# Kernel tuning notes

Measured on AMD Instinct MI355X. Metric: run time of the kernel, lower is better.

## Reference

```python
import jax, jax.numpy as jnp
import numpy as np


def setup_inputs() -> dict:
    key = jax.random.key(0)
    k1, k2, k3, k4 = jax.random.split(key, 4)
    B, N, dim, heads, dim_head = 4, 1025, 768, 12, 64
    inner = heads * dim_head
    x = jax.random.normal(k1, (B, N, dim), dtype=jnp.float32)
    # binary occlusion mask over the N-1 patch tokens (CLS handled inside forward)
    mask = (jax.random.uniform(k2, (B, N - 1, dim)) > 0.5).astype(jnp.float32)
    w_qkv = jax.random.normal(k3, (inner * 3, dim), dtype=jnp.float32) * 0.02
    w_out = jax.random.normal(k4, (dim, inner), dtype=jnp.float32) * 0.02
    b_out = jnp.zeros((dim,), dtype=jnp.float32)
    return {"x": x, "mask": mask, "w_qkv": w_qkv, "w_out": w_out, "b_out": b_out, "heads": heads}


def reference(x, mask, w_qkv, w_out, b_out, heads):
    B, N, dim = x.shape
    inner = w_qkv.shape[0] // 3
    d = inner // heads
    scale = d ** -0.5

    def split_heads(t):  # [B, n, h*d] -> [B, h, n, d]
        return t.reshape(B, t.shape[1], heads, d).transpose(0, 2, 1, 3)

    qkv = x @ w_qkv.T  # [B, N, 3*inner]
    q, k, v = map(split_heads, jnp.split(qkv, 3, axis=-1))

    # --- mask propagation (torch.no_grad block) ---
    mask_sg = jax.lax.stop_gradient(mask)
    qkv_m = mask_sg @ jax.lax.stop_gradient(jnp.abs(w_qkv)).T  # [B, N-1, 3*inner]

    def norm_mask(t):
        t = split_heads(t)  # [B, h, N-1, d]
        t = t / (1e-6 + jnp.max(t, axis=2, keepdims=True))
        return jnp.concatenate([jnp.ones_like(t[:, :, :1]), t], axis=2)  # [B, h, N, d]

    q_m, k_m, v_m = map(norm_mask, jnp.split(qkv_m, 3, axis=-1))
    updated = (jnp.mean(mask_sg, axis=-1, keepdims=True) > 0.0).astype(x.dtype)  # [B, N-1, 1]
    updated = jnp.concatenate([jnp.ones_like(updated[:, :1]), updated], axis=1)  # [B, N, 1]

    # --- masked attention ---
    dots = jnp.einsum('bhnd,bhmd->bhnm', q * q_m, k * k_m) * scale
    attn = jax.nn.softmax(dots, axis=-1)
    out = jnp.einsum('bhnm,bhmd->bhnd', attn, v_m * v)
    out = out.transpose(0, 2, 1, 3).reshape(B, N, inner) * updated
    out = out @ w_out.T + b_out

    # --- mask output propagation (no grad) ---
    m = jax.lax.stop_gradient(jnp.einsum('bhnm,bhmd->bhnd', attn, v_m))
    m = m.transpose(0, 2, 1, 3).reshape(B, N, inner) * updated
    m = m @ jax.lax.stop_gradient(jnp.abs(w_out)).T
    return (out, m[:, 1:])
```

## Files before the change

kernel.cpp:

```cpp
#include <hip/hip_runtime.h>
#include <cmath>

#define TPB 256

static const int NTOK  = 1025;
static const int DIM   = 768;
static const int HEADS = 12;
static const int QK3   = 2304;
static const int ROWS  = 4 * NTOK;
static const int MROWS = 4 * (NTOK - 1);
static const int MPAD  = 4224;
static const int NPAD  = 1088;
static const size_t OUT0 = (size_t)ROWS * DIM;
static const size_t APLANE = (size_t)MPAD * DIM;

static const size_t OFF_QKV16  = 0;
static const size_t OFF_QKVM16 = 4800000;
static const size_t OFF_QE     = 9600000;
static const size_t OFF_KF     = 11300000;
static const size_t OFF_VF     = 13000000;
static const size_t OFF_ABF    = 16400000;
static const size_t OFF_WQ     = 19700000;
static const size_t OFF_WO     = 21500000;
static const size_t OFF_CMAX   = 22100000;
static const size_t OFF_UPD    = 22110000;

typedef __attribute__((ext_vector_type(8))) short short8;
typedef __attribute__((ext_vector_type(4))) float f32x4;

__device__ __forceinline__ unsigned short f2bf(float f) {
    union { float f; unsigned int u; } c; c.f = f;
    unsigned int u = c.u + 0x7fffu + ((c.u >> 16) & 1u);
    return (unsigned short)(u >> 16);
}
__device__ __forceinline__ float bf2f(unsigned short u) {
    union { unsigned int u; float f; } c; c.u = (unsigned int)u << 16;
    return c.f;
}
__device__ __forceinline__ unsigned int cvtpk(float a, float b) {
    unsigned int r;
    asm("v_cvt_pk_bf16_f32 %0, %1, %2" : "=v"(r) : "v"(a), "v"(b));
    return r;
}
__device__ __forceinline__ void gl_lds16(const unsigned short* g, unsigned short* l) {
    __builtin_amdgcn_global_load_lds(
        (const __attribute__((address_space(1))) unsigned int*)g,
        (__attribute__((address_space(3))) unsigned int*)l, 16, 0, 0);
}

__global__ __launch_bounds__(TPB)
void k_cvt(const float* __restrict__ x, const float* __restrict__ mask,
           const float* __restrict__ wqkv, const float* __restrict__ wout,
           unsigned short* __restrict__ Abf, unsigned short* __restrict__ Wq,
           unsigned short* __restrict__ Wo, float* __restrict__ upd,
           float* __restrict__ cmax)
{
    const int z = blockIdx.z;
    if (z == 4) {
        const int bx = blockIdx.x;
        if (bx == 0) {
            if (threadIdx.x < 4) upd[threadIdx.x * NTOK] = 1.f;
        } else if (bx < 10) {
            const int i4 = (bx - 1) * 256 + threadIdx.x;
            *(float4*)(cmax + (size_t)i4 * 4) = (float4){0.f, 0.f, 0.f, 0.f};
        }
        return;
    }
    const size_t idx = ((size_t)blockIdx.x * TPB + threadIdx.x) * 8;
    union { unsigned int u[4]; short8 s; } pk;
    if (z <= 1) {
        if (idx >= APLANE) return;
        const int row = (int)(idx / DIM);
        const int M = z ? MROWS : ROWS;
        const float* src = z ? mask : x;
        if (row < M) {
            float a[8];
            *(float4*)&a[0] = *(const float4*)(src + idx);
            *(float4*)&a[4] = *(const float4*)(src + idx + 4);
            pk.u[0] = cvtpk(a[0], a[1]); pk.u[1] = cvtpk(a[2], a[3]);
            pk.u[2] = cvtpk(a[4], a[5]); pk.u[3] = cvtpk(a[6], a[7]);
            if (z == 1) {
                const float s = ((a[0] + a[1]) + (a[2] + a[3])) + ((a[4] + a[5]) + (a[6] + a[7]));
                if (s > 0.f) {
                    const int b = row >> 10, j = row & 1023;
                    upd[b * NTOK + j + 1] = 1.f;
                }
            }
        } else {
            pk.u[0] = pk.u[1] = pk.u[2] = pk.u[3] = 0u;
        }
        *(short8*)(Abf + (size_t)z * APLANE + idx) = pk.s;
    } else {
        const size_t tot = (z == 2) ? (size_t)QK3 * DIM : (size_t)DIM * DIM;
        if (idx >= tot) return;
        const float* src = (z == 2) ? wqkv : wout;
        unsigned short* dst = (z == 2) ? Wq : Wo;
        float a[8];
        *(float4*)&a[0] = *(const float4*)(src + idx);
        *(float4*)&a[4] = *(const float4*)(src + idx + 4);
        union { unsigned int u[4]; short8 s; } pa;
        pk.u[0] = cvtpk(a[0], a[1]); pk.u[1] = cvtpk(a[2], a[3]);
        pk.u[2] = cvtpk(a[4], a[5]); pk.u[3] = cvtpk(a[6], a[7]);
#pragma unroll
        for (int i = 0; i < 4; ++i) pa.u[i] = pk.u[i] & 0x7FFF7FFFu;
        *(short8*)(dst + idx) = pk.s;
        *(short8*)(dst + tot + idx) = pa.s;
    }
}

__global__ __launch_bounds__(TPB)
void k_gemm_qkv_mfma(const unsigned short* __restrict__ Abf,
                     const unsigned short* __restrict__ Wq,
                     unsigned short* __restrict__ qkv16,
                     unsigned short* __restrict__ qkvm16,
                     float* __restrict__ cmax)
{
    const int bid = blockIdx.x;
    const int xcd = bid & 7, rr = bid >> 3;
    const int id = (xcd < 4) ? (xcd * 149 + rr) : (596 + (xcd - 4) * 148 + rr);
    const int z = id / 594;
    const int rem = id - z * 594;
    const int by = rem / 18, bx = rem - by * 18;
    const int rowT = by * 128, colT = bx * 128;
    if (z == 1 && rowT >= MROWS) return;
    const unsigned short* A = Abf + (size_t)z * APLANE;
    const unsigned short* B = Wq + (size_t)z * QK3 * DIM;

    __shared__ unsigned short As[2][128 * 64];
    __shared__ unsigned short Bs[2][128 * 64];

    const int t = threadIdx.x;
    const int w = t >> 6, lane = t & 63, l15 = lane & 15, quad = lane >> 4;
    const int wm = (w & 1) * 64, wn = (w >> 1) * 64;

    auto stage = [&](int buf, int k0) {
#pragma unroll
        for (int p = 0; p < 4; ++p) {
            const int i = p * 256 + t;
            const int row = i >> 3, ch = i & 7;
            const int gc = k0 + ((ch ^ (row & 7)) << 3);
            gl_lds16(A + (size_t)(rowT + row) * DIM + gc, As[buf] + (size_t)i * 8);
            gl_lds16(B + (size_t)(colT + row) * DIM + gc, Bs[buf] + (size_t)i * 8);
        }
    };

    f32x4 acc[4][4];
#pragma unroll
    for (int i = 0; i < 4; ++i)
#pragma unroll
        for (int j = 0; j < 4; ++j) acc[i][j] = (f32x4){0.f, 0.f, 0.f, 0.f};

    stage(0, 0);
#pragma clang loop unroll(disable)
    for (int kt = 0; kt < 12; ++kt) {
        const int cur = kt & 1;
        if (kt < 11) {
            stage(cur ^ 1, (kt + 1) * 64);
            asm volatile("s_waitcnt vmcnt(8)" ::: "memory");
        } else {
            asm volatile("s_waitcnt vmcnt(0)" ::: "memory");
        }
        __builtin_amdgcn_s_barrier();
        __builtin_amdgcn_sched_barrier(0);
        const unsigned short* as = As[cur];
        const unsigned short* bs = Bs[cur];
        short8 fa[2][4], fb[2][4];
#pragma unroll
        for (int kk = 0; kk < 2; ++kk) {
            const int rc = ((kk * 4 + quad) ^ (l15 & 7)) << 3;
#pragma unroll
            for (int mi = 0; mi < 4; ++mi) {
                fa[kk][mi] = *(const short8*)(as + (wm + mi * 16 + l15) * 64 + rc);
                fb[kk][mi] = *(const short8*)(bs + (wn + mi * 16 + l15) * 64 + rc);
            }
        }
        __builtin_amdgcn_s_setprio(1);
#pragma unroll
        for (int kk = 0; kk < 2; ++kk)
#pragma unroll
            for (int mi = 0; mi < 4; ++mi)
#pragma unroll
                for (int ni = 0; ni < 4; ++ni)
                    acc[mi][ni] = __builtin_amdgcn_mfma_f32_16x16x32_bf16(fa[kk][mi], fb[kk][ni], acc[mi][ni], 0, 0, 0);
        __builtin_amdgcn_s_setprio(0);
        asm volatile("s_waitcnt lgkmcnt(0)" ::: "memory");
        __builtin_amdgcn_s_barrier();
    }

    float cm[4] = {0.f, 0.f, 0.f, 0.f};
#pragma unroll
    for (int mi = 0; mi < 4; ++mi)
#pragma unroll
        for (int ni = 0; ni < 4; ++ni) {
            const int col = colT + wn + ni * 16 + l15;
#pragma unroll
            for (int r = 0; r < 4; ++r) {
                const int row = rowT + wm + mi * 16 + quad * 4 + r;
                const float v = acc[mi][ni][r];
                if (z == 0) {
                    if (row < ROWS) qkv16[(size_t)row * QK3 + col] = f2bf(v);
                } else {
                    qkvm16[(size_t)row * QK3 + col] = f2bf(v);
                    cm[ni] = fmaxf(cm[ni], v);
                }
            }
        }
    if (z == 1) {
        const int bb = rowT >> 10;
#pragma unroll
        for (int ni = 0; ni < 4; ++ni) {
            float m = cm[ni];
            m = fmaxf(m, __shfl_xor(m, 16, 64));
            m = fmaxf(m, __shfl_xor(m, 32, 64));
            if (quad == 0)
                atomicMax((int*)&cmax[bb * QK3 + colT + wn + ni * 16 + l15], __float_as_int(m));
        }
    }
}

__global__ __launch_bounds__(TPB)
void k_prep(const unsigned short* __restrict__ qkv16,
            const unsigned short* __restrict__ qkvm16,
            const float* __restrict__ cmax, unsigned short* __restrict__ qe,
            unsigned short* __restrict__ kfrag, unsigned short* __restrict__ vfrag)
{
    __shared__ unsigned short Vt_l[128 * 66];
    const int t = threadIdx.x;
    const int nt = blockIdx.x, h = blockIdx.y, b = blockIdx.z;
    const int bh = b * HEADS + h;
    const int nl = t >> 2, ds0 = (t & 3) * 16;
    const int n = nt * 64 + nl;
    const bool valid = n < NTOK;
    const int col0 = h * 64 + ds0;

    unsigned short q16[16] __attribute__((aligned(16))) = {0};
    unsigned short k16[16] __attribute__((aligned(16))) = {0};
    unsigned short v16[16] __attribute__((aligned(16))) = {0};
    unsigned short qm16[16] __attribute__((aligned(16)));
    unsigned short km16[16] __attribute__((aligned(16)));
    unsigned short vm16[16] __attribute__((aligned(16)));
    float cq[16], ck[16], cv[16];

    const bool useM = valid && (n > 0);
    if (valid) {
        const size_t br = (size_t)(b * NTOK + n) * QK3 + col0;
        *(short8*)&q16[0] = *(const short8*)(qkv16 + br);
        *(short8*)&q16[8] = *(const short8*)(qkv16 + br + 8);
        *(short8*)&k16[0] = *(const short8*)(qkv16 + br + 768);
        *(short8*)&k16[8] = *(const short8*)(qkv16 + br + 776);
        *(short8*)&v16[0] = *(const short8*)(qkv16 + br + 1536);
        *(short8*)&v16[8] = *(const short8*)(qkv16 + br + 1544);
    }
    if (useM) {
        const size_t mr = (size_t)(b * 1024 + (n - 1)) * QK3 + col0;
        *(short8*)&qm16[0] = *(const short8*)(qkvm16 + mr);
        *(short8*)&qm16[8] = *(const short8*)(qkvm16 + mr + 8);
        *(short8*)&km16[0] = *(const short8*)(qkvm16 + mr + 768);
        *(short8*)&km16[8] = *(const short8*)(qkvm16 + mr + 776);
        *(short8*)&vm16[0] = *(const short8*)(qkvm16 + mr + 1536);
        *(short8*)&vm16[8] = *(const short8*)(qkvm16 + mr + 1544);
        const int cb = b * QK3 + col0;
#pragma unroll
        for (int i = 0; i < 4; ++i) {
            *(float4*)&cq[i * 4] = *(const float4*)(cmax + cb + i * 4);
            *(float4*)&ck[i * 4] = *(const float4*)(cmax + cb + 768 + i * 4);
            *(float4*)&cv[i * 4] = *(const float4*)(cmax + cb + 1536 + i * 4);
        }
    }

    float fq[16], fk[16];
#pragma unroll
    for (int idx = 0; idx < 16; ++idx) {
        const float qm = useM ? bf2f(qm16[idx]) / (1e-6f + cq[idx]) : 1.f;
        const float km = useM ? bf2f(km16[idx]) / (1e-6f + ck[idx]) : 1.f;
        const float vm = valid ? (useM ? bf2f(vm16[idx]) / (1e-6f + cv[idx]) : 1.f) : 0.f;
        fq[idx] = bf2f(q16[idx]) * qm * 0.18033688f;
        fk[idx] = bf2f(k16[idx]) * km;
        const int d = ds0 + idx;
        Vt_l[d * 66 + nl]        = f2bf(bf2f(v16[idx]) * vm);
        Vt_l[(64 + d) * 66 + nl] = f2bf(vm);
    }
    union { unsigned int u[4]; short8 s; } pq0, pq1, pk0, pk1;
#pragma unroll
    for (int i = 0; i < 4; ++i) {
        pq0.u[i] = cvtpk(fq[2 * i],     fq[2 * i + 1]);
        pq1.u[i] = cvtpk(fq[8 + 2 * i], fq[9 + 2 * i]);
        pk0.u[i] = cvtpk(fk[2 * i],     fk[2 * i + 1]);
        pk1.u[i] = cvtpk(fk[8 + 2 * i], fk[9 + 2 * i]);
    }
    {
        unsigned short* qp = qe + ((size_t)bh * NPAD + n) * 64 + ds0;
        *(short8*)qp       = pq0.s;
        *(short8*)(qp + 8) = pq1.s;
    }
    {
        const int nc = nl >> 4, l15 = nl & 15;
        const int kk = ds0 >> 5, qb = (ds0 & 31) >> 3;
        unsigned short* kp = kfrag + (((size_t)bh * 17 + nt) * 8 + kk * 4 + nc) * 512;
        *(short8*)(kp + ((size_t)(qb * 16 + l15)) * 8)       = pk0.s;
        *(short8*)(kp + ((size_t)((qb + 1) * 16 + l15)) * 8) = pk1.s;
    }
    __syncthreads();
    const int c = t >> 1, nh = (t & 1) * 32;
    unsigned short ov[32] __attribute__((aligned(16)));
#pragma unroll
    for (int i = 0; i < 32; ++i) ov[i] = Vt_l[c * 66 + nh + i];
    const int c8 = c >> 4, l15v = c & 15, kkv = nh >> 5;
    unsigned short* vp = vfrag + (((size_t)bh * 17 + nt) * 16 + c8 * 2 + kkv) * 512 + (size_t)l15v * 8;
#pragma unroll
    for (int qd = 0; qd < 4; ++qd)
        *(short8*)(vp + (size_t)qd * 128) = *(short8*)(ov + qd * 8);
}

__global__ __launch_bounds__(64, 2)
void k_attn(const unsigned short* __restrict__ qe, const unsigned short* __restrict__ kfrag,
            const unsigned short* __restrict__ vfrag, const float* __restrict__ upd,
            unsigned short* __restrict__ ab2)
{
    const int flat = blockIdx.y * 33 + blockIdx.x;
    const int d2 = (flat & 7) * 198 + (flat >> 3);
    const int bh = d2 / 33, qt = d2 - bh * 33;
    const int b = bh / HEADS, h = bh - b * HEADS;
    const int lane = threadIdx.x;
    const int l15 = lane & 15, quad = lane >> 4;
    const int q0 = qt * 32;

    short8 qf[2][2];
#pragma unroll
    for (int j = 0; j < 2; ++j) {
        const unsigned short* qp = qe + ((size_t)bh * NPAD + q0 + j * 16 + l15) * 64 + (quad << 3);
        qf[j][0] = *(const short8*)qp;
        qf[j][1] = *(const short8*)(qp + 32);
    }
    const int pA = (quad & 1) * 32 + l15;
    const int pB = pA + 16;
    const bool lo32 = (lane < 32);

    const unsigned short* kb = kfrag + (size_t)bh * (17 * 8 * 512) + (size_t)lane * 8;
    const unsigned short* vb = vfrag + (size_t)bh * (17 * 16 * 512) + (size_t)lane * 8;

    short8 kf[8], vf[16];
#pragma unroll
    for (int g = 0; g < 8; ++g) kf[g] = *(const short8*)(kb + g * 512);
#pragma unroll
    for (int g = 0; g < 16; ++g) vf[g] = *(const short8*)(vb + g * 512);

    f32x4 acc[2][8];
    float lac[2] = {0.f, 0.f};
#pragma unroll
    for (int j = 0; j < 2; ++j)
#pragma unroll
        for (int g = 0; g < 8; ++g) acc[j][g] = (f32x4){0.f, 0.f, 0.f, 0.f};

    const float EC = 14.4269504f;

#pragma clang loop unroll(disable)
    for (int kt = 0; kt < 17; ++kt) {
        f32x4 s[2][4];
        __builtin_amdgcn_s_setprio(1);
#pragma unroll
        for (int nc = 0; nc < 4; ++nc) {
#pragma unroll
            for (int j = 0; j < 2; ++j) {
                f32x4 z = (f32x4){0.f, 0.f, 0.f, 0.f};
                z = __builtin_amdgcn_mfma_f32_16x16x32_bf16(kf[nc], qf[j][0], z, 0, 0, 0);
                z = __builtin_amdgcn_mfma_f32_16x16x32_bf16(kf[4 + nc], qf[j][1], z, 0, 0, 0);
                s[j][nc] = z;
            }
        }
        __builtin_amdgcn_s_setprio(0);
        if (kt < 16) {
            const unsigned short* kn = kb + (size_t)(kt + 1) * 4096;
#pragma unroll
            for (int g = 0; g < 8; ++g) kf[g] = *(const short8*)(kn + g * 512);
        }
        short8 pf[2][2];
#pragma unroll
        for (int j = 0; j < 2; ++j) {
            unsigned int dA[4], dB[4];
            float psum = 0.f, p00 = 0.f;
#pragma unroll
            for (int nc = 0; nc < 4; ++nc) {
                const float p0 = __builtin_amdgcn_exp2f(s[j][nc][0] - EC);
                const float p1 = __builtin_amdgcn_exp2f(s[j][nc][1] - EC);
                const float p2 = __builtin_amdgcn_exp2f(s[j][nc][2] - EC);
                const float p3 = __builtin_amdgcn_exp2f(s[j][nc][3] - EC);
                dA[nc] = cvtpk(p0, p1);
                dB[nc] = cvtpk(p2, p3);
                psum += (p0 + p1) + (p2 + p3);
                if (nc == 0) p00 = p0;
            }
            if (kt < 16) lac[j] += psum;
            else if (quad == 0) lac[j] += p00;
            union { int i[4]; short8 s; } u0, u1;
            {
                const int a0 = __shfl((int)dA[0], pA, 64), a1 = __shfl((int)dA[1], pA, 64);
                const int b0 = __shfl((int)dB[0], pA, 64), b1 = __shfl((int)dB[1], pA, 64);
                const int a2 = __shfl((int)dA[0], pB, 64), a3 = __shfl((int)dA[1], pB, 64);
                const int b2 = __shfl((int)dB[0], pB, 64), b3 = __shfl((int)dB[1], pB, 64);
                u0.i[0] = lo32 ? a0 : a1;
                u0.i[1] = lo32 ? b0 : b1;
                u0.i[2] = lo32 ? a2 : a3;
                u0.i[3] = lo32 ? b2 : b3;
            }
            {
                const int a0 = __shfl((int)dA[2], pA, 64), a1 = __shfl((int)dA[3], pA, 64);
                const int b0 = __shfl((int)dB[2], pA, 64), b1 = __shfl((int)dB[3], pA, 64);
                const int a2 = __shfl((int)dA[2], pB, 64), a3 = __shfl((int)dA[3], pB, 64);
                const int b2 = __shfl((int)dB[2], pB, 64), b3 = __shfl((int)dB[3], pB, 64);
                u1.i[0] = lo32 ? a0 : a1;
                u1.i[1] = lo32 ? b0 : b1;
                u1.i[2] = lo32 ? a2 : a3;
                u1.i[3] = lo32 ? b2 : b3;
            }
            pf[j][0] = u0.s;
            pf[j][1] = u1.s;
        }
        __builtin_amdgcn_s_setprio(1);
#pragma unroll
        for (int g = 0; g < 8; ++g) {
#pragma unroll
            for (int j = 0; j < 2; ++j) {
                acc[j][g] = __builtin_amdgcn_mfma_f32_16x16x32_bf16(vf[2 * g],     pf[j][0], acc[j][g], 0, 0, 0);
                acc[j][g] = __builtin_amdgcn_mfma_f32_16x16x32_bf16(vf[2 * g + 1], pf[j][1], acc[j][g], 0, 0, 0);
            }
        }
        __builtin_amdgcn_s_setprio(0);
        if (kt < 16) {
            const unsigned short* vn = vb + (size_t)(kt + 1) * 8192;
#pragma unroll
            for (int g = 0; g < 16; ++g) vf[g] = *(const short8*)(vn + g * 512);
        }
    }

#pragma unroll
    for (int j = 0; j < 2; ++j) {
        float lq = lac[j];
        lq += __shfl_xor(lq, 16, 64);
        lq += __shfl_xor(lq, 32, 64);
        const int qrow = q0 + j * 16 + l15;
        if (qrow < NTOK) {
            const size_t rg = (size_t)b * NTOK + qrow;
            const float inv = upd[rg] / lq;
#pragma unroll
            for (int g = 0; g < 8; ++g) {
                uint2 pk;
                pk.x = cvtpk(acc[j][g][0] * inv, acc[j][g][1] * inv);
                pk.y = cvtpk(acc[j][g][2] * inv, acc[j][g][3] * inv);
                const size_t addr = (size_t)(g >> 2) * APLANE + rg * DIM + h * 64 + (g & 3) * 16 + quad * 4;
                *(uint2*)(ab2 + addr) = pk;
            }
        }
    }
}

__global__ __launch_bounds__(TPB)
void k_gemm_out_mfma(const unsigned short* __restrict__ ab2,
                     const unsigned short* __restrict__ Wo,
                     const float* __restrict__ bout, float* __restrict__ dout)
{
    const int bid = blockIdx.x;
    const int xcd = bid & 7, rr = bid >> 3;
    const int id = xcd * 99 + rr;
    const int z = id / 396;
    const int rem = id - z * 396;
    const int by = rem / 12, bx = rem - by * 12;
    const int rowT = by * 128, colT = bx * 64;

    const unsigned short* A = ab2 + (size_t)z * APLANE;
    const unsigned short* B = Wo + (size_t)z * DIM * DIM;

    __shared__ unsigned short As[2][128 * 64];
    __shared__ unsigned short Bs[2][64 * 64];

    const int t = threadIdx.x;
    const int w = t >> 6, lane = t & 63, l15 = lane & 15, quad = lane >> 4;
    const int wm = (w & 1) * 64, wn = (w >> 1) * 32;

    auto stage = [&](int buf, int k0) {
#pragma unroll
        for (int p = 0; p < 4; ++p) {
            const int i = p * 256 + t;
            const int row = i >> 3, ch = i & 7;
            const int gc = k0 + ((ch ^ (row & 7)) << 3);
            gl_lds16(A + (size_t)(rowT + row) * DIM + gc, As[buf] + (size_t)i * 8);
        }
#pragma unroll
        for (int p = 0; p < 2; ++p) {
            const int i = p * 256 + t;
            const int row = i >> 3, ch = i & 7;
            const int gc = k0 + ((ch ^ (row & 7)) << 3);
            gl_lds16(B + (size_t)(colT + row) * DIM + gc, Bs[buf] + (size_t)i * 8);
        }
    };

    f32x4 acc[4][2];
#pragma unroll
    for (int i = 0; i < 4; ++i)
#pragma unroll
        for (int j = 0; j < 2; ++j) acc[i][j] = (f32x4){0.f, 0.f, 0.f, 0.f};

    stage(0, 0);
#pragma clang loop unroll(disable)
    for (int kt = 0; kt < 12; ++kt) {
        const int cur = kt & 1;
        if (kt < 11) {
            stage(cur ^ 1, (kt + 1) * 64);
            asm volatile("s_waitcnt vmcnt(6)" ::: "memory");
        } else {
            asm volatile("s_waitcnt vmcnt(0)" ::: "memory");
        }
        __builtin_amdgcn_s_barrier();
        __builtin_amdgcn_sched_barrier(0);
        const unsigned short* as = As[cur];
        const unsigned short* bs = Bs[cur];
        short8 fa[2][4], fb[2][2];
#pragma unroll
        for (int kk = 0; kk < 2; ++kk) {
            const int rc = ((kk * 4 + quad) ^ (l15 & 7)) << 3;
#pragma unroll
            for (int mi = 0; mi < 4; ++mi)
                fa[kk][mi] = *(const short8*)(as + (wm + mi * 16 + l15) * 64 + rc);
#pragma unroll
            for (int ni = 0; ni < 2; ++ni)
                fb[kk][ni] = *(const short8*)(bs + (wn + ni * 16 + l15) * 64 + rc);
        }
        __builtin_amdgcn_s_setprio(1);
#pragma unroll
        for (int kk = 0; kk < 2; ++kk)
#pragma unroll
            for (int mi = 0; mi < 4; ++mi)
#pragma unroll
                for (int ni = 0; ni < 2; ++ni)
                    acc[mi][ni] = __builtin_amdgcn_mfma_f32_16x16x32_bf16(fa[kk][mi], fb[kk][ni], acc[mi][ni], 0, 0, 0);
        __builtin_amdgcn_s_setprio(0);
        asm volatile("s_waitcnt lgkmcnt(0)" ::: "memory");
        __builtin_amdgcn_s_barrier();
    }

#pragma unroll
    for (int mi = 0; mi < 4; ++mi)
#pragma unroll
        for (int ni = 0; ni < 2; ++ni) {
            const int col = colT + wn + ni * 16 + l15;
            const float bb = (z == 0) ? bout[col] : 0.f;
#pragma unroll
            for (int r = 0; r < 4; ++r) {
                const int row = rowT + wm + mi * 16 + quad * 4 + r;
                if (row >= ROWS) continue;
                const int b = row / NTOK, n = row % NTOK;
                if (z == 0) {
                    dout[(size_t)row * DIM + col] = acc[mi][ni][r] + bb;
                } else if (n >= 1) {
                    dout[OUT0 + ((size_t)(b * (NTOK - 1) + (n - 1))) * DIM + col] = acc[mi][ni][r];
                }
            }
        }
}

extern "C" void kernel_launch(void* const* d_in, const int* in_sizes, int n_in,
                              void* d_out, int out_size, void* d_ws, size_t ws_size,
                              hipStream_t stream)
{
    const float* x    = (const float*)d_in[0];
    const float* mask = (const float*)d_in[1];
    const float* wqkv = (const float*)d_in[2];
    const float* wout = (const float*)d_in[3];
    const float* bout = (const float*)d_in[4];
    float* ws = (float*)d_ws;
    unsigned short* qkv16  = (unsigned short*)(ws + OFF_QKV16);
    unsigned short* qkvm16 = (unsigned short*)(ws + OFF_QKVM16);
    unsigned short* qe  = (unsigned short*)(ws + OFF_QE);
    unsigned short* kfr = (unsigned short*)(ws + OFF_KF);
    unsigned short* vfr = (unsigned short*)(ws + OFF_VF);
    unsigned short* abf = (unsigned short*)(ws + OFF_ABF);
    unsigned short* wq  = (unsigned short*)(ws + OFF_WQ);
    unsigned short* wo  = (unsigned short*)(ws + OFF_WO);
    float* cmax = ws + OFF_CMAX;
    float* upd  = ws + OFF_UPD;
    float* out  = (float*)d_out;

    hipMemsetAsync(upd, 0, ROWS * sizeof(float), stream);
    hipLaunchKernelGGL(k_cvt,           dim3(1584, 1, 5), dim3(TPB), 0, stream, x, mask, wqkv, wout, abf, wq, wo, upd, cmax);
    hipLaunchKernelGGL(k_gemm_qkv_mfma, dim3(1188),       dim3(TPB), 0, stream, abf, wq, qkv16, qkvm16, cmax);
    hipLaunchKernelGGL(k_prep,          dim3(17, 12, 4),  dim3(TPB), 0, stream, qkv16, qkvm16, cmax, qe, kfr, vfr);
    hipLaunchKernelGGL(k_attn,          dim3(33, 48),     dim3(64),  0, stream, qe, kfr, vfr, upd, abf);
    hipLaunchKernelGGL(k_gemm_out_mfma, dim3(792),        dim3(TPB), 0, stream, abf, wo, bout, out);
}
```

Before: 217.7 us.

## Halve attention query tile to 16 rows and widen output GEMM tile to 128x128

```diff
diff --git a/kernel.cpp b/kernel.cpp
--- a/kernel.cpp
+++ b/kernel.cpp
@@ -317,20 +317,19 @@
             const unsigned short* __restrict__ vfrag, const float* __restrict__ upd,
             unsigned short* __restrict__ ab2)
 {
-    const int flat = blockIdx.y * 33 + blockIdx.x;
-    const int d2 = (flat & 7) * 198 + (flat >> 3);
-    const int bh = d2 / 33, qt = d2 - bh * 33;
+    const int flat = blockIdx.y * 66 + blockIdx.x;
+    const int d2 = (flat & 7) * 396 + (flat >> 3);
+    const int bh = d2 / 66, qt = d2 - bh * 66;
     const int b = bh / HEADS, h = bh - b * HEADS;
     const int lane = threadIdx.x;
     const int l15 = lane & 15, quad = lane >> 4;
-    const int q0 = qt * 32;
-
-    short8 qf[2][2];
-#pragma unroll
-    for (int j = 0; j < 2; ++j) {
-        const unsigned short* qp = qe + ((size_t)bh * NPAD + q0 + j * 16 + l15) * 64 + (quad << 3);
-        qf[j][0] = *(const short8*)qp;
-        qf[j][1] = *(const short8*)(qp + 32);
+    const int q0 = qt * 16;
+
+    short8 qf0, qf1;
+    {
+        const unsigned short* qp = qe + ((size_t)bh * NPAD + q0 + l15) * 64 + (quad << 3);
+        qf0 = *(const short8*)qp;
+        qf1 = *(const short8*)(qp + 32);
     }
     const int pA = (quad & 1) * 32 + l15;
     const int pB = pA + 16;
@@ -345,28 +344,23 @@
 #pragma unroll
     for (int g = 0; g < 16; ++g) vf[g] = *(const short8*)(vb + g * 512);
 
-    f32x4 acc[2][8];
-    float lac[2] = {0.f, 0.f};
-#pragma unroll
-    for (int j = 0; j < 2; ++j)
-#pragma unroll
-        for (int g = 0; g < 8; ++g) acc[j][g] = (f32x4){0.f, 0.f, 0.f, 0.f};
+    f32x4 acc[8];
+    float lac = 0.f;
+#pragma unroll
+    for (int g = 0; g < 8; ++g) acc[g] = (f32x4){0.f, 0.f, 0.f, 0.f};
 
     const float EC = 14.4269504f;
 
 #pragma clang loop unroll(disable)
     for (int kt = 0; kt < 17; ++kt) {
-        f32x4 s[2][4];
+        f32x4 s[4];
         __builtin_amdgcn_s_setprio(1);
 #pragma unroll
         for (int nc = 0; nc < 4; ++nc) {
-#pragma unroll
-            for (int j = 0; j < 2; ++j) {
-                f32x4 z = (f32x4){0.f, 0.f, 0.f, 0.f};
-                z = __builtin_amdgcn_mfma_f32_16x16x32_bf16(kf[nc], qf[j][0], z, 0, 0, 0);
-                z = __builtin_amdgcn_mfma_f32_16x16x32_bf16(kf[4 + nc], qf[j][1], z, 0, 0, 0);
-                s[j][nc] = z;
-            }
+            f32x4 z = (f32x4){0.f, 0.f, 0.f, 0.f};
+            z = __builtin_amdgcn_mfma_f32_16x16x32_bf16(kf[nc], qf0, z, 0, 0, 0);
+            z = __builtin_amdgcn_mfma_f32_16x16x32_bf16(kf[4 + nc], qf1, z, 0, 0, 0);
+            s[nc] = z;
         }
         __builtin_amdgcn_s_setprio(0);
         if (kt < 16) {
@@ -374,24 +368,23 @@
 #pragma unroll
             for (int g = 0; g < 8; ++g) kf[g] = *(const short8*)(kn + g * 512);
         }
-        short8 pf[2][2];
-#pragma unroll
-        for (int j = 0; j < 2; ++j) {
+        short8 pf0, pf1;
+        {
             unsigned int dA[4], dB[4];
             float psum = 0.f, p00 = 0.f;
 #pragma unroll
             for (int nc = 0; nc < 4; ++nc) {
-                const float p0 = __builtin_amdgcn_exp2f(s[j][nc][0] - EC);
-                const float p1 = __builtin_amdgcn_exp2f(s[j][nc][1] - EC);
-                const float p2 = __builtin_amdgcn_exp2f(s[j][nc][2] - EC);
-                const float p3 = __builtin_amdgcn_exp2f(s[j][nc][3] - EC);
+                const float p0 = __builtin_amdgcn_exp2f(s[nc][0] - EC);
+                const float p1 = __builtin_amdgcn_exp2f(s[nc][1] - EC);
+                const float p2 = __builtin_amdgcn_exp2f(s[nc][2] - EC);
+                const float p3 = __builtin_amdgcn_exp2f(s[nc][3] - EC);
                 dA[nc] = cvtpk(p0, p1);
                 dB[nc] = cvtpk(p2, p3);
                 psum += (p0 + p1) + (p2 + p3);
                 if (nc == 0) p00 = p0;
             }
-            if (kt < 16) lac[j] += psum;
-            else if (quad == 0) lac[j] += p00;
+            if (kt < 16) lac += psum;
+            else if (quad == 0) lac += p00;
             union { int i[4]; short8 s; } u0, u1;
             {
                 const int a0 = __shfl((int)dA[0], pA, 64), a1 = __shfl((int)dA[1], pA, 64);
@@ -413,17 +406,14 @@
                 u1.i[2] = lo32 ? a2 : a3;
                 u1.i[3] = lo32 ? b2 : b3;
             }
-            pf[j][0] = u0.s;
-            pf[j][1] = u1.s;
+            pf0 = u0.s;
+            pf1 = u1.s;
         }
         __builtin_amdgcn_s_setprio(1);
 #pragma unroll
         for (int g = 0; g < 8; ++g) {
-#pragma unroll
-            for (int j = 0; j < 2; ++j) {
-                acc[j][g] = __builtin_amdgcn_mfma_f32_16x16x32_bf16(vf[2 * g],     pf[j][0], acc[j][g], 0, 0, 0);
-                acc[j][g] = __builtin_amdgcn_mfma_f32_16x16x32_bf16(vf[2 * g + 1], pf[j][1], acc[j][g], 0, 0, 0);
-            }
+            acc[g] = __builtin_amdgcn_mfma_f32_16x16x32_bf16(vf[2 * g],     pf0, acc[g], 0, 0, 0);
+            acc[g] = __builtin_amdgcn_mfma_f32_16x16x32_bf16(vf[2 * g + 1], pf1, acc[g], 0, 0, 0);
         }
         __builtin_amdgcn_s_setprio(0);
         if (kt < 16) {
@@ -433,20 +423,19 @@
         }
     }
 
-#pragma unroll
-    for (int j = 0; j < 2; ++j) {
-        float lq = lac[j];
+    {
+        float lq = lac;
         lq += __shfl_xor(lq, 16, 64);
         lq += __shfl_xor(lq, 32, 64);
-        const int qrow = q0 + j * 16 + l15;
+        const int qrow = q0 + l15;
         if (qrow < NTOK) {
             const size_t rg = (size_t)b * NTOK + qrow;
             const float inv = upd[rg] / lq;
 #pragma unroll
             for (int g = 0; g < 8; ++g) {
                 uint2 pk;
-                pk.x = cvtpk(acc[j][g][0] * inv, acc[j][g][1] * inv);
-                pk.y = cvtpk(acc[j][g][2] * inv, acc[j][g][3] * inv);
+                pk.x = cvtpk(acc[g][0] * inv, acc[g][1] * inv);
+                pk.y = cvtpk(acc[g][2] * inv, acc[g][3] * inv);
                 const size_t addr = (size_t)(g >> 2) * APLANE + rg * DIM + h * 64 + (g & 3) * 16 + quad * 4;
                 *(uint2*)(ab2 + addr) = pk;
             }
@@ -461,21 +450,21 @@
 {
     const int bid = blockIdx.x;
     const int xcd = bid & 7, rr = bid >> 3;
-    const int id = xcd * 99 + rr;
-    const int z = id / 396;
-    const int rem = id - z * 396;
-    const int by = rem / 12, bx = rem - by * 12;
-    const int rowT = by * 128, colT = bx * 64;
+    const int id = (xcd < 4) ? (xcd * 50 + rr) : (200 + (xcd - 4) * 49 + rr);
+    const int z = id / 198;
+    const int rem = id - z * 198;
+    const int by = rem / 6, bx = rem - by * 6;
+    const int rowT = by * 128, colT = bx * 128;
 
     const unsigned short* A = ab2 + (size_t)z * APLANE;
     const unsigned short* B = Wo + (size_t)z * DIM * DIM;
 
     __shared__ unsigned short As[2][128 * 64];
-    __shared__ unsigned short Bs[2][64 * 64];
+    __shared__ unsigned short Bs[2][128 * 64];
 
     const int t = threadIdx.x;
     const int w = t >> 6, lane = t & 63, l15 = lane & 15, quad = lane >> 4;
-    const int wm = (w & 1) * 64, wn = (w >> 1) * 32;
+    const int wm = (w & 1) * 64, wn = (w >> 1) * 64;
 
     auto stage = [&](int buf, int k0) {
 #pragma unroll
@@ -484,21 +473,15 @@
             const int row = i >> 3, ch = i & 7;
             const int gc = k0 + ((ch ^ (row & 7)) << 3);
             gl_lds16(A + (size_t)(rowT + row) * DIM + gc, As[buf] + (size_t)i * 8);
-        }
-#pragma unroll
-        for (int p = 0; p < 2; ++p) {
-            const int i = p * 256 + t;
-            const int row = i >> 3, ch = i & 7;
-            const int gc = k0 + ((ch ^ (row & 7)) << 3);
             gl_lds16(B + (size_t)(colT + row) * DIM + gc, Bs[buf] + (size_t)i * 8);
         }
     };
 
-    f32x4 acc[4][2];
+    f32x4 acc[4][4];
 #pragma unroll
     for (int i = 0; i < 4; ++i)
 #pragma unroll
-        for (int j = 0; j < 2; ++j) acc[i][j] = (f32x4){0.f, 0.f, 0.f, 0.f};
+        for (int j = 0; j < 4; ++j) acc[i][j] = (f32x4){0.f, 0.f, 0.f, 0.f};
 
     stage(0, 0);
 #pragma clang loop unroll(disable)
@@ -506,7 +489,7 @@
         const int cur = kt & 1;
         if (kt < 11) {
             stage(cur ^ 1, (kt + 1) * 64);
-            asm volatile("s_waitcnt vmcnt(6)" ::: "memory");
+            asm volatile("s_waitcnt vmcnt(8)" ::: "memory");
         } else {
             asm volatile("s_waitcnt vmcnt(0)" ::: "memory");
         }
@@ -514,24 +497,23 @@
         __builtin_amdgcn_sched_barrier(0);
         const unsigned short* as = As[cur];
         const unsigned short* bs = Bs[cur];
-        short8 fa[2][4], fb[2][2];
+        short8 fa[2][4], fb[2][4];
 #pragma unroll
         for (int kk = 0; kk < 2; ++kk) {
             const int rc = ((kk * 4 + quad) ^ (l15 & 7)) << 3;
 #pragma unroll
+            for (int mi = 0; mi < 4; ++mi) {
+                fa[kk][mi] = *(const short8*)(as + (wm + mi * 16 + l15) * 64 + rc);
+                fb[kk][mi] = *(const short8*)(bs + (wn + mi * 16 + l15) * 64 + rc);
+            }
+        }
+        __builtin_amdgcn_s_setprio(1);
+#pragma unroll
+        for (int kk = 0; kk < 2; ++kk)
+#pragma unroll
             for (int mi = 0; mi < 4; ++mi)
-                fa[kk][mi] = *(const short8*)(as + (wm + mi * 16 + l15) * 64 + rc);
-#pragma unroll
-            for (int ni = 0; ni < 2; ++ni)
-                fb[kk][ni] = *(const short8*)(bs + (wn + ni * 16 + l15) * 64 + rc);
-        }
-        __builtin_amdgcn_s_setprio(1);
-#pragma unroll
-        for (int kk = 0; kk < 2; ++kk)
-#pragma unroll
-            for (int mi = 0; mi < 4; ++mi)
-#pragma unroll
-                for (int ni = 0; ni < 2; ++ni)
+#pragma unroll
+                for (int ni = 0; ni < 4; ++ni)
                     acc[mi][ni] = __builtin_amdgcn_mfma_f32_16x16x32_bf16(fa[kk][mi], fb[kk][ni], acc[mi][ni], 0, 0, 0);
         __builtin_amdgcn_s_setprio(0);
         asm volatile("s_waitcnt lgkmcnt(0)" ::: "memory");
@@ -541,7 +523,7 @@
 #pragma unroll
     for (int mi = 0; mi < 4; ++mi)
 #pragma unroll
-        for (int ni = 0; ni < 2; ++ni) {
+        for (int ni = 0; ni < 4; ++ni) {
             const int col = colT + wn + ni * 16 + l15;
             const float bb = (z == 0) ? bout[col] : 0.f;
 #pragma unroll
@@ -584,6 +566,6 @@
     hipLaunchKernelGGL(k_cvt,           dim3(1584, 1, 5), dim3(TPB), 0, stream, x, mask, wqkv, wout, abf, wq, wo, upd, cmax);
     hipLaunchKernelGGL(k_gemm_qkv_mfma, dim3(1188),       dim3(TPB), 0, stream, abf, wq, qkv16, qkvm16, cmax);
     hipLaunchKernelGGL(k_prep,          dim3(17, 12, 4),  dim3(TPB), 0, stream, qkv16, qkvm16, cmax, qe, kfr, vfr);
-    hipLaunchKernelGGL(k_attn,          dim3(33, 48),     dim3(64),  0, stream, qe, kfr, vfr, upd, abf);
-    hipLaunchKernelGGL(k_gemm_out_mfma, dim3(792),        dim3(TPB), 0, stream, abf, wo, bout, out);
-}
+    hipLaunchKernelGGL(k_attn,          dim3(66, 48),     dim3(64),  0, stream, qe, kfr, vfr, upd, abf);
+    hipLaunchKernelGGL(k_gemm_out_mfma, dim3(396),        dim3(TPB), 0, stream, abf, wo, bout, out);
+}
```

Result: slower. 228.4 us (+4.9%).
